# Kernel tuning notes

Hardware: AMD Instinct MI355X
Metric: run time of the kernel (lower is better)

The kernel has to match this reference:

```python
import jax, jax.numpy as jnp
import numpy as np

N_FFT = 512
HOP = 128
WIN = 512
BATCH = 32
N_SAMPLES = 480000


def make_forward_basis():
    n_freq = N_FFT // 2 + 1  # 257
    # periodic hann window (torch.hann_window default periodic=True)
    n = np.arange(WIN, dtype=np.float32)
    window = 0.5 * (1.0 - np.cos(2.0 * np.pi * n / WIN))
    freqs = np.linspace(0.0, N_FFT // 2, n_freq, dtype=np.float32)  # [n_freq]
    t = np.arange(WIN, dtype=np.float32)
    phase = 2.0 * np.pi * freqs[:, None] * t[None, :] / N_FFT
    real = np.cos(phase) * window[None, :]
    imag = -np.sin(phase) * window[None, :]
    basis = np.concatenate([real, imag], axis=0)[:, None, :]
    return jnp.asarray(basis, dtype=jnp.float32)


def setup_inputs() -> dict:
    key = jax.random.key(0)
    x = jax.random.normal(key, (BATCH, N_SAMPLES), dtype=jnp.float32)
    return {"x": x, "forward_basis": make_forward_basis()}


def reference(x, forward_basis):
    # x: [B, T] -> [B, 1, T]
    x = x[:, None, :]
    pad = N_FFT // 2
    x_padded = jnp.pad(x, ((0, 0), (0, 0), (pad, pad)), mode="reflect")
    # single conv over concatenated real+imag basis: [B, 2*n_freq, n_frames]
    spec = jax.lax.conv_general_dilated(
        x_padded, forward_basis,
        window_strides=(HOP,), padding="VALID",
        dimension_numbers=("NCH", "OIH", "NCH"))
    n_freq = N_FFT // 2 + 1
    real_spec = spec[:, :n_freq, :]
    imag_spec = spec[:, n_freq:, :]
    return jnp.sqrt(real_spec ** 2 + imag_spec ** 2)
```

## Files before the change

kernel.cpp:

```cpp
#include <hip/hip_runtime.h>

#define NFREQ   257
#define NFRAMES 3751
#define NS      480000
#define HOP     128
#define WIN     512

#define NB      32
#define BN      128
#define NFT     30
#define STEPS   32
#define XWPITCH 272
#define XW_B    35632
#define AHALF   16384
#define WNYQ_B  2048
#define XGROUPS 2096

typedef __attribute__((ext_vector_type(8))) short short8;
typedef __attribute__((ext_vector_type(4))) float f32x4;

__device__ __forceinline__ short f2bf(float f) {
    __bf16 b = (__bf16)f;
    return __builtin_bit_cast(short, b);
}
__device__ __forceinline__ float bf2f(short s) {
    unsigned int u = ((unsigned int)(unsigned short)s) << 16;
    return __builtin_bit_cast(float, u);
}
__device__ __forceinline__ void gload_lds16(const void* g, void* l) {
    __builtin_amdgcn_global_load_lds(
        (const __attribute__((address_space(1))) void*)g,
        (__attribute__((address_space(3))) void*)l, 16, 0, 0);
}

__global__ __launch_bounds__(256)
void prep_basis9(const float* __restrict__ basis,
                 short* __restrict__ abL, short* __restrict__ wnyqG) {
    int g = blockIdx.x * 256 + threadIdx.x;
    if (g < 32768) {
        int ob   = g * 16;
        int step = ob >> 14;
        int w    = (ob >> 12) & 3;
        int pl   = (ob >> 11) & 1;
        int m    = (ob >> 10) & 1;
        int lane = (ob >> 4) & 63;
        int l15  = lane & 15;
        int lgrp = lane >> 4;
        int fr   = (step >> 4) * 128 + w * 32 + m * 16 + l15;
        int k0   = (step & 15) * 32 + lgrp * 8;
        const float4* p = reinterpret_cast<const float4*>(
            basis + ((size_t)(pl * NFREQ + fr)) * WIN + k0);
        float4 a0 = p[0], a1 = p[1];
        short8 v;
        v[0]=f2bf(a0.x); v[1]=f2bf(a0.y); v[2]=f2bf(a0.z); v[3]=f2bf(a0.w);
        v[4]=f2bf(a1.x); v[5]=f2bf(a1.y); v[6]=f2bf(a1.z); v[7]=f2bf(a1.w);
        *reinterpret_cast<short8*>(reinterpret_cast<char*>(abL) + ob) = v;
    } else if (g < 32832) {
        int j = g - 32768;
        const float4* p = reinterpret_cast<const float4*>(basis + (size_t)256 * WIN + j * 8);
        float4 a0 = p[0], a1 = p[1];
        short8 v;
        v[0]=f2bf(a0.x); v[1]=f2bf(a0.y); v[2]=f2bf(a0.z); v[3]=f2bf(a0.w);
        v[4]=f2bf(a1.x); v[5]=f2bf(a1.y); v[6]=f2bf(a1.z); v[7]=f2bf(a1.w);
        *reinterpret_cast<short8*>(wnyqG + j * 8) = v;
    }
}

__global__ __launch_bounds__(256, 2)
void stft_mfma_kernel(const float* __restrict__ x,
                      const short* __restrict__ abL,
                      const short* __restrict__ wnyqG,
                      float* __restrict__ out)
{
    __shared__ __align__(16) char smem[XW_B + 2 * AHALF + WNYQ_B];
    char* const xw   = smem;
    char* const aBuf = smem + XW_B;
    float* const wny = reinterpret_cast<float*>(smem + XW_B + 2 * AHALF);

    const int tid  = threadIdx.x;
    const int wave = tid >> 6;
    const int lane = tid & 63;
    const int lgrp = lane >> 4;
    const int l15  = lane & 15;

    const int logical = (blockIdx.x & 7) * 120 + (blockIdx.x >> 3);
    const int ft = logical % NFT;
    const int b  = logical / NFT;
    const int t0 = ft * BN;

    const char* abLc = (const char*)abL;
    const int wBase = wave * 4096;

    #pragma unroll
    for (int i = 0; i < 4; ++i)
        gload_lds16(abLc + wBase + i * 1024 + lane * 16,
                    aBuf + wBase + i * 1024);
    {
        short a0 = wnyqG[tid * 2], a1 = wnyqG[tid * 2 + 1];
        wny[tid * 2]     = bf2f(a0);
        wny[tid * 2 + 1] = bf2f(a1);
    }

    {
        const float* __restrict__ xb = x + (size_t)b * NS;
        const int sbase = t0 * 128 - 256;
        #pragma unroll
        for (int i = 0; i < 9; ++i) {
            int g = tid + i * 256;
            if (g < XGROUPS) {
                int ix = sbase + g * 8;
                short8 v;
                if (ix >= 0 && ix + 8 <= NS) {
                    const float4* p = reinterpret_cast<const float4*>(xb + ix);
                    float4 a0 = p[0], a1 = p[1];
                    v[0]=f2bf(a0.x); v[1]=f2bf(a0.y); v[2]=f2bf(a0.z); v[3]=f2bf(a0.w);
                    v[4]=f2bf(a1.x); v[5]=f2bf(a1.y); v[6]=f2bf(a1.z); v[7]=f2bf(a1.w);
                } else {
                    #pragma unroll
                    for (int q = 0; q < 8; ++q) {
                        int idx = ix + q;
                        if (idx < 0) idx = -idx;
                        if (idx >= NS + 256) { v[q] = 0; continue; }
                        if (idx >= NS) idx = 2 * NS - 2 - idx;
                        v[q] = f2bf(xb[idx]);
                    }
                }
                *reinterpret_cast<short8*>(xw + (g >> 4) * XWPITCH + (g & 15) * 16) = v;
            }
        }
    }
    __syncthreads();

    f32x4 accR[2][8], accI[2][8];
    #pragma unroll
    for (int m = 0; m < 2; ++m)
        #pragma unroll
        for (int n = 0; n < 8; ++n) {
            accR[m][n] = f32x4{0.f,0.f,0.f,0.f};
            accI[m][n] = f32x4{0.f,0.f,0.f,0.f};
        }

    const int aPerm = lane * 16;

    const int nfl = wave * 32 + (lane & 31);
    const int nh  = lane >> 5;
    const int nyqXbase = (nfl + 2 * nh) * XWPITCH;
    const float* const nyqW = wny + nh * 256;
    float nacc = 0.f;

    #pragma unroll 1
    for (int s = 0; s < STEPS; ++s) {
        asm volatile("s_waitcnt vmcnt(0)" ::: "memory");
        __builtin_amdgcn_sched_barrier(0);

        if (s + 1 < STEPS) {
            const char* sb = abLc + (size_t)(s + 1) * AHALF + wBase;
            char* dst = aBuf + ((s + 1) & 1) * AHALF + wBase;
            #pragma unroll
            for (int i = 0; i < 4; ++i)
                gload_lds16(sb + i * 1024 + lane * 16, dst + i * 1024);
        }
        __builtin_amdgcn_sched_barrier(0);

        const int ks32 = s & 15;
        const char* aCur = aBuf + (s & 1) * AHALF + wBase;
        short8 aRv[2], aIv[2], xv[8];
        #pragma unroll
        for (int m = 0; m < 2; ++m) {
            aRv[m] = *reinterpret_cast<const short8*>(aCur + m * 1024 + aPerm);
            aIv[m] = *reinterpret_cast<const short8*>(aCur + 2048 + m * 1024 + aPerm);
        }
        {
            int r8 = ks32 * 64 + lgrp * 16;
            int T  = r8 + ((r8 >> 8) << 4);
            const char* xwl = xw + l15 * XWPITCH + T;
            #pragma unroll
            for (int nt = 0; nt < 8; ++nt)
                xv[nt] = *reinterpret_cast<const short8*>(xwl + nt * (16 * XWPITCH));
        }
        #pragma unroll
        for (int m = 0; m < 2; ++m)
            #pragma unroll
            for (int nt = 0; nt < 8; ++nt) {
                accR[m][nt] = __builtin_amdgcn_mfma_f32_16x16x32_bf16(aRv[m], xv[nt], accR[m][nt], 0, 0, 0);
                accI[m][nt] = __builtin_amdgcn_mfma_f32_16x16x32_bf16(aIv[m], xv[nt], accI[m][nt], 0, 0, 0);
            }

        {
            short8 nx = *reinterpret_cast<const short8*>(
                xw + nyqXbase + (s >> 4) * XWPITCH + (s & 15) * 16);
            const float* wrow = nyqW + s * 8;
            #pragma unroll
            for (int q = 0; q < 8; ++q)
                nacc = fmaf(bf2f(nx[q]), wrow[q], nacc);
        }

        if ((s & 15) == 15) {
            const int fp = s >> 4;
            float* ob = out + (size_t)b * NFREQ * NFRAMES;
            const int fb = fp * 128 + wave * 32 + lgrp * 4;
            const int tb = t0 + l15;
            #pragma unroll
            for (int m = 0; m < 2; ++m)
                #pragma unroll
                for (int nt = 0; nt < 8; ++nt) {
                    int t = tb + nt * 16;
                    if (t < NFRAMES) {
                        #pragma unroll
                        for (int r = 0; r < 4; ++r) {
                            int f = fb + m * 16 + r;
                            float vr = accR[m][nt][r], vi = accI[m][nt][r];
                            ob[(size_t)f * NFRAMES + t] =
                                __builtin_amdgcn_sqrtf(vr * vr + vi * vi);
                        }
                    }
                    accR[m][nt] = f32x4{0.f,0.f,0.f,0.f};
                    accI[m][nt] = f32x4{0.f,0.f,0.f,0.f};
                }
        }
    }

    {
        nacc += __shfl_xor(nacc, 32);
        int t = t0 + nfl;
        if (nh == 0 && t < NFRAMES)
            out[((size_t)b * NFREQ + 256) * NFRAMES + t] = fabsf(nacc);
    }
}

extern "C" void kernel_launch(void* const* d_in, const int* in_sizes, int n_in,
                              void* d_out, int out_size, void* d_ws, size_t ws_size,
                              hipStream_t stream) {
    const float* x     = (const float*)d_in[0];
    const float* basis = (const float*)d_in[1];
    float* out = (float*)d_out;

    short* abL   = (short*)d_ws;
    short* wnyqG = abL + 262144;

    prep_basis9<<<dim3(129), 256, 0, stream>>>(basis, abL, wnyqG);
    stft_mfma_kernel<<<dim3(NFT * NB), 256, 0, stream>>>(x, abL, wnyqG, out);
}
```

Measured before the change: 77.57 us.

## Load basis fragments straight into registers with a register double buffer

Drops the LDS double buffer for the pre-permuted bf16 basis, which was filled with global_load_lds and guarded by a full vmcnt(0) wait every step. Each lane now reads its A fragments directly from global memory into registers, one step ahead, using two register sets in a loop unrolled by two. This frees 32 KB of LDS and the per-step waits and LDS reads, but adds registers and exposes global or L2 latency if the one-step prefetch cannot hide it.

```diff
diff --git a/kernel.cpp b/kernel.cpp
--- a/kernel.cpp
+++ b/kernel.cpp
@@ -12,7 +12,6 @@
 #define STEPS   32
 #define XWPITCH 272
 #define XW_B    35632
-#define AHALF   16384
 #define WNYQ_B  2048
 #define XGROUPS 2096
 
@@ -26,11 +25,6 @@
 __device__ __forceinline__ float bf2f(short s) {
     unsigned int u = ((unsigned int)(unsigned short)s) << 16;
     return __builtin_bit_cast(float, u);
-}
-__device__ __forceinline__ void gload_lds16(const void* g, void* l) {
-    __builtin_amdgcn_global_load_lds(
-        (const __attribute__((address_space(1))) void*)g,
-        (__attribute__((address_space(3))) void*)l, 16, 0, 0);
 }
 
 __global__ __launch_bounds__(256)
@@ -72,10 +66,9 @@
                       const short* __restrict__ wnyqG,
                       float* __restrict__ out)
 {
-    __shared__ __align__(16) char smem[XW_B + 2 * AHALF + WNYQ_B];
+    __shared__ __align__(16) char smem[XW_B + WNYQ_B];
     char* const xw   = smem;
-    char* const aBuf = smem + XW_B;
-    float* const wny = reinterpret_cast<float*>(smem + XW_B + 2 * AHALF);
+    float* const wny = reinterpret_cast<float*>(smem + XW_B);
 
     const int tid  = threadIdx.x;
     const int wave = tid >> 6;
@@ -88,13 +81,8 @@
     const int b  = logical / NFT;
     const int t0 = ft * BN;
 
-    const char* abLc = (const char*)abL;
-    const int wBase = wave * 4096;
-
-    #pragma unroll
-    for (int i = 0; i < 4; ++i)
-        gload_lds16(abLc + wBase + i * 1024 + lane * 16,
-                    aBuf + wBase + i * 1024);
+    const char* const aS = (const char*)abL + (wave << 12) + lane * 16;
+
     {
         short a0 = wnyqG[tid * 2], a1 = wnyqG[tid * 2 + 1];
         wny[tid * 2]     = bf2f(a0);
@@ -140,84 +128,86 @@
             accI[m][n] = f32x4{0.f,0.f,0.f,0.f};
         }
 
-    const int aPerm = lane * 16;
-
     const int nfl = wave * 32 + (lane & 31);
     const int nh  = lane >> 5;
     const int nyqXbase = (nfl + 2 * nh) * XWPITCH;
     const float* const nyqW = wny + nh * 256;
     float nacc = 0.f;
 
+    short8 R0[2], I0[2], R1[2], I1[2];
+
+    #define ALOAD(RS, IS, s)                                                        \
+    {                                                                               \
+        const char* p_ = aS + (size_t)(s) * 16384;                                  \
+        (RS)[0] = *reinterpret_cast<const short8*>(p_);                             \
+        (RS)[1] = *reinterpret_cast<const short8*>(p_ + 1024);                      \
+        (IS)[0] = *reinterpret_cast<const short8*>(p_ + 2048);                      \
+        (IS)[1] = *reinterpret_cast<const short8*>(p_ + 3072);                      \
+    }
+
+    #define COMPUTE(s, R, I)                                                        \
+    {                                                                               \
+        short8 xv[8];                                                               \
+        {                                                                           \
+            int r8 = ((s) & 15) * 64 + lgrp * 16;                                   \
+            int T  = r8 + ((r8 >> 8) << 4);                                         \
+            const char* xwl = xw + l15 * XWPITCH + T;                               \
+            _Pragma("unroll")                                                       \
+            for (int nt = 0; nt < 8; ++nt)                                          \
+                xv[nt] = *reinterpret_cast<const short8*>(xwl + nt * (16 * XWPITCH)); \
+        }                                                                           \
+        _Pragma("unroll")                                                           \
+        for (int m = 0; m < 2; ++m)                                                 \
+            _Pragma("unroll")                                                       \
+            for (int nt = 0; nt < 8; ++nt) {                                        \
+                accR[m][nt] = __builtin_amdgcn_mfma_f32_16x16x32_bf16(              \
+                    (R)[m], xv[nt], accR[m][nt], 0, 0, 0);                          \
+                accI[m][nt] = __builtin_amdgcn_mfma_f32_16x16x32_bf16(              \
+                    (I)[m], xv[nt], accI[m][nt], 0, 0, 0);                          \
+            }                                                                       \
+        {                        \
+            short8 nx = *reinterpret_cast<const short8*>(                           \
+                xw + nyqXbase + ((s) >> 4) * XWPITCH + ((s) & 15) * 16);            \
+            const float* wrow = nyqW + (s) * 8;                                     \
+            _Pragma("unroll")                                                       \
+            for (int q = 0; q < 8; ++q)                                             \
+                nacc = fmaf(bf2f(nx[q]), wrow[q], nacc);                            \
+        }                                                                           \
+    }
+
+    #define EPILOGUE(fp)                                                            \
+    {                                                                               \
+        float* ob = out + (size_t)b * NFREQ * NFRAMES;                              \
+        const int fb = (fp) * 128 + wave * 32 + lgrp * 4;                           \
+        const int tb = t0 + l15;                                                    \
+        _Pragma("unroll")                                                           \
+        for (int m = 0; m < 2; ++m)                                                 \
+            _Pragma("unroll")                                                       \
+            for (int nt = 0; nt < 8; ++nt) {                                        \
+                int t = tb + nt * 16;                                               \
+                if (t < NFRAMES) {                                                  \
+                    _Pragma("unroll")                                               \
+                    for (int r = 0; r < 4; ++r) {                                   \
+                        int f = fb + m * 16 + r;                                    \
+                        float vr = accR[m][nt][r], vi = accI[m][nt][r];             \
+                        ob[(size_t)f * NFRAMES + t] =                               \
+                            __builtin_amdgcn_sqrtf(vr * vr + vi * vi);              \
+                    }                                                               \
+                }                                                                   \
+                accR[m][nt] = f32x4{0.f,0.f,0.f,0.f};                               \
+                accI[m][nt] = f32x4{0.f,0.f,0.f,0.f};                               \
+            }                                                                       \
+    }
+
+    ALOAD(R0, I0, 0);
+
     #pragma unroll 1
-    for (int s = 0; s < STEPS; ++s) {
-        asm volatile("s_waitcnt vmcnt(0)" ::: "memory");
-        __builtin_amdgcn_sched_barrier(0);
-
-        if (s + 1 < STEPS) {
-            const char* sb = abLc + (size_t)(s + 1) * AHALF + wBase;
-            char* dst = aBuf + ((s + 1) & 1) * AHALF + wBase;
-            #pragma unroll
-            for (int i = 0; i < 4; ++i)
-                gload_lds16(sb + i * 1024 + lane * 16, dst + i * 1024);
-        }
-        __builtin_amdgcn_sched_barrier(0);
-
-        const int ks32 = s & 15;
-        const char* aCur = aBuf + (s & 1) * AHALF + wBase;
-        short8 aRv[2], aIv[2], xv[8];
-        #pragma unroll
-        for (int m = 0; m < 2; ++m) {
-            aRv[m] = *reinterpret_cast<const short8*>(aCur + m * 1024 + aPerm);
-            aIv[m] = *reinterpret_cast<const short8*>(aCur + 2048 + m * 1024 + aPerm);
-        }
-        {
-            int r8 = ks32 * 64 + lgrp * 16;
-            int T  = r8 + ((r8 >> 8) << 4);
-            const char* xwl = xw + l15 * XWPITCH + T;
-            #pragma unroll
-            for (int nt = 0; nt < 8; ++nt)
-                xv[nt] = *reinterpret_cast<const short8*>(xwl + nt * (16 * XWPITCH));
-        }
-        #pragma unroll
-        for (int m = 0; m < 2; ++m)
-            #pragma unroll
-            for (int nt = 0; nt < 8; ++nt) {
-                accR[m][nt] = __builtin_amdgcn_mfma_f32_16x16x32_bf16(aRv[m], xv[nt], accR[m][nt], 0, 0, 0);
-                accI[m][nt] = __builtin_amdgcn_mfma_f32_16x16x32_bf16(aIv[m], xv[nt], accI[m][nt], 0, 0, 0);
-            }
-
-        {
-            short8 nx = *reinterpret_cast<const short8*>(
-                xw + nyqXbase + (s >> 4) * XWPITCH + (s & 15) * 16);
-            const float* wrow = nyqW + s * 8;
-            #pragma unroll
-            for (int q = 0; q < 8; ++q)
-                nacc = fmaf(bf2f(nx[q]), wrow[q], nacc);
-        }
-
-        if ((s & 15) == 15) {
-            const int fp = s >> 4;
-            float* ob = out + (size_t)b * NFREQ * NFRAMES;
-            const int fb = fp * 128 + wave * 32 + lgrp * 4;
-            const int tb = t0 + l15;
-            #pragma unroll
-            for (int m = 0; m < 2; ++m)
-                #pragma unroll
-                for (int nt = 0; nt < 8; ++nt) {
-                    int t = tb + nt * 16;
-                    if (t < NFRAMES) {
-                        #pragma unroll
-                        for (int r = 0; r < 4; ++r) {
-                            int f = fb + m * 16 + r;
-                            float vr = accR[m][nt][r], vi = accI[m][nt][r];
-                            ob[(size_t)f * NFRAMES + t] =
-                                __builtin_amdgcn_sqrtf(vr * vr + vi * vi);
-                        }
-                    }
-                    accR[m][nt] = f32x4{0.f,0.f,0.f,0.f};
-                    accI[m][nt] = f32x4{0.f,0.f,0.f,0.f};
-                }
-        }
+    for (int s = 0; s < STEPS; s += 2) {
+        ALOAD(R1, I1, s + 1);
+        COMPUTE(s, R0, I0);
+        if (s + 2 < STEPS) ALOAD(R0, I0, s + 2);
+        COMPUTE(s + 1, R1, I1);
+        if ((s & 15) == 14) EPILOGUE(s >> 4);
     }
 
     {
```

Result: faster. 73.88 us (-4.8%).
